# Performance work log

Measured on AMD Instinct MI355X. Metric: run time of the kernel, lower is better.

Reference implementation:

```python
import jax, jax.numpy as jnp
import numpy as np

T, H, I, E, Z, TOPK = 1024, 1024, 512, 32, 8, 4
ROUTED_SCALING = 1.0


def setup_inputs() -> dict:
    key = jax.random.key(0)
    k1, k2, k3, k4 = jax.random.split(key, 4)
    return {
        "hidden_states": jax.random.normal(k1, (T, H), jnp.float32),
        "router_w": jax.random.normal(k2, (E + Z, H), jnp.float32) * 0.02,
        "correction_bias": jnp.zeros((E + Z,), jnp.float32),
        "w_gate_up": jax.random.normal(k3, (E, 2 * I, H), jnp.float32) * 0.02,
        "w_down": jax.random.normal(k4, (E, H, I), jnp.float32) * 0.02,
        "top_k": TOPK,
    }


def reference(hidden_states, router_w, correction_bias, w_gate_up, w_down, top_k):
    # hidden_states: [T, H]; router_w: [E+Z, H]; w_gate_up: [E, 2I, H]; w_down: [E, H, I]
    t, h = hidden_states.shape
    e = w_gate_up.shape[0]
    i = w_down.shape[2]
    # --- router (float32, no bias; correction bias only affects selection) ---
    logits = jnp.einsum("th,eh->te", hidden_states.astype(jnp.float32), router_w)
    scores = jax.nn.softmax(logits, axis=-1)                     # [T, E+Z]
    _, idx = jax.lax.top_k(scores + correction_bias[None, :], top_k)  # [T, k]
    w = jnp.take_along_axis(scores, idx, axis=1) * ROUTED_SCALING     # renormalize=False
    # combine matrix [T, E+Z] (sparse top-k scattered dense)
    comb = jnp.zeros((t, scores.shape[1]), jnp.float32)
    comb = comb.at[jnp.arange(t)[:, None], idx].add(w)
    comb_routed = comb[:, :e].astype(hidden_states.dtype)        # [T, E]
    zero_w = comb[:, e:].sum(-1).astype(hidden_states.dtype)     # [T] identity zero-experts
    # --- grouped SiLU-gated expert MLPs (dense all-experts reference) ---
    gu = jnp.einsum("th,eih->eti", hidden_states, w_gate_up)     # [E, T, 2I]
    hmid = jax.nn.silu(gu[..., :i]) * gu[..., i:]                # [E, T, I]
    ye = jnp.einsum("eti,ehi->eth", hmid, w_down)                # [E, T, H]
    out = jnp.einsum("te,eth->th", comb_routed, ye)
    out = out + zero_w[:, None] * hidden_states
    return out
```

## Files before the change

kernel.cpp:

```cpp
#include <hip/hip_runtime.h>
#include <hip/hip_bf16.h>
#include <math.h>

#define TT   1024
#define HH   1024
#define II   512
#define EE   32
#define NE   40
#define TOPK 4
#define CAP  1024

#define GM  128
#define GK  32

typedef __attribute__((ext_vector_type(4))) short short4v;
typedef __attribute__((ext_vector_type(8))) short short8v;
typedef __attribute__((ext_vector_type(4))) float floatx4;

static __device__ __forceinline__ short f2bf(float f) {
    unsigned u = __float_as_uint(f);
    unsigned r = (u + 0x7fffu + ((u >> 16) & 1u)) >> 16;
    return (short)(r & 0xffffu);
}
static __device__ __forceinline__ float bf2f(short s) {
    return __uint_as_float(((unsigned)(unsigned short)s) << 16);
}
#if defined(__has_builtin)
#if __has_builtin(__builtin_amdgcn_cvt_pk_bf16_f32)
#define HAVE_PK_BF16 1
#endif
#endif
static __device__ __forceinline__ unsigned pk2(float a, float b) {
#ifdef HAVE_PK_BF16
    typedef __attribute__((ext_vector_type(2))) __bf16 bf2t;
    union { bf2t v; unsigned u; } cv;
    cv.v = __builtin_amdgcn_cvt_pk_bf16_f32(a, b);
    return cv.u;
#else
    return (unsigned)(unsigned short)f2bf(a) | ((unsigned)(unsigned short)f2bf(b) << 16);
#endif
}
static __device__ __forceinline__ short4v cvt4(float4 v) {
    union { unsigned u[2]; short4v s; } cv;
    cv.u[0] = pk2(v.x, v.y); cv.u[1] = pk2(v.z, v.w);
    return cv.s;
}
static __device__ __forceinline__ short8v pack8(float4 f0, float4 f1) {
    union { short4v h[2]; short8v v; } u;
    u.h[0] = cvt4(f0); u.h[1] = cvt4(f1);
    return u.v;
}


__global__ __launch_bounds__(256, 4) void kA(
    const float* __restrict__ x, const float* __restrict__ rw,
    const float* __restrict__ bias, float* __restrict__ topk_w,
    float* __restrict__ zero_w, int* __restrict__ kexp,
    short* __restrict__ xb)
{
    const int bx = blockIdx.x, tid = threadIdx.x;
    const int lane = tid & 63;
    const int w    = tid >> 6;

    if (w < 2) {
        const int t = bx * 2 + w;
        float xv[16];
        #pragma unroll
        for (int i = 0; i < 16; ++i) xv[i] = x[(size_t)t * HH + 64 * i + lane];

        float mylogit = -INFINITY;
        for (int e0 = 0; e0 < NE; e0 += 4) {
            const float* r0 = rw + (size_t)e0 * HH;
            float p[4] = { 0.f, 0.f, 0.f, 0.f };
            #pragma unroll
            for (int i = 0; i < 16; ++i) {
                int h = 64 * i + lane;
                #pragma unroll
                for (int j = 0; j < 4; ++j) p[j] += xv[i] * r0[(size_t)j * HH + h];
            }
            #pragma unroll
            for (int j = 0; j < 4; ++j) {
                #pragma unroll
                for (int off = 32; off > 0; off >>= 1) p[j] += __shfl_xor(p[j], off);
                if (lane == e0 + j) mylogit = p[j];
            }
        }

        float m = mylogit;
        #pragma unroll
        for (int off = 32; off > 0; off >>= 1) m = fmaxf(m, __shfl_xor(m, off));
        float pexp = (lane < NE) ? expf(mylogit - m) : 0.f;
        float s = pexp;
        #pragma unroll
        for (int off = 32; off > 0; off >>= 1) s += __shfl_xor(s, off);
        const float score = pexp / s;

        float val = (lane < NE) ? score + bias[lane] : -INFINITY;
        int   kidx[TOPK];
        float kw[TOPK];
        #pragma unroll
        for (int k = 0; k < TOPK; ++k) {
            float v = val; int idx = lane;
            #pragma unroll
            for (int off = 32; off > 0; off >>= 1) {
                float ov = __shfl_xor(v, off);
                int   oi = __shfl_xor(idx, off);
                if (ov > v || (ov == v && oi < idx)) { v = ov; idx = oi; }
            }
            kidx[k] = idx;
            kw[k]   = __shfl(score, idx);
            if (lane == idx) val = -INFINITY;
        }

        if (lane == 0) {
            float zw = 0.f;
            #pragma unroll
            for (int k = 0; k < TOPK; ++k) {
                int slot = t * TOPK + k;
                topk_w[slot] = kw[k];
                kexp[slot]   = kidx[k];
                if (kidx[k] >= EE) zw += kw[k];
            }
            zero_w[t] = zw;
        }
    } else {
        const int t = bx * 2 + (w - 2);
        const float4* xr = (const float4*)(x + (size_t)t * HH);
        short4v* xbr = (short4v*)(xb + (size_t)t * HH);
        #pragma unroll
        for (int i = 0; i < 4; ++i) xbr[lane + 64 * i] = cvt4(xr[lane + 64 * i]);
    }
}

__global__ __launch_bounds__(256, 4) void kA2(
    const int* __restrict__ kexp, int* __restrict__ counts,
    int* __restrict__ slots)
{
    __shared__ int wsum[4];
    __shared__ int base;
    const int e = blockIdx.x;
    const int tid = threadIdx.x, lane = tid & 63, w = tid >> 6;
    if (tid == 0) base = 0;
    __syncthreads();
    for (int i0 = 0; i0 < TT * TOPK; i0 += 256) {
        const int i = i0 + tid;
        const bool m = (kexp[i] == e);
        unsigned long long bal = __ballot(m);
        int pre  = __popcll(bal & ((1ull << lane) - 1ull));
        int wcnt = __popcll(bal);
        if (lane == 0) wsum[w] = wcnt;
        __syncthreads();
        int woff = 0;
        #pragma unroll
        for (int j = 0; j < 4; ++j) if (j < w) woff += wsum[j];
        const int tot = wsum[0] + wsum[1] + wsum[2] + wsum[3];
        if (m) slots[e * CAP + base + woff + pre] = i;
        __syncthreads();
        if (tid == 0) base += tot;
        __syncthreads();
    }
    if (tid == 0) counts[e] = base;
}

__global__ __launch_bounds__(256, 4) void kB(
    const short* __restrict__ xb, const float* __restrict__ wgu,
    const int* __restrict__ counts, const int* __restrict__ slots,
    const float* __restrict__ topk_w, short* __restrict__ hmid)
{
    __shared__ int   ssl[GM];
    __shared__ float swv[GM];
    const int bx = blockIdx.x, tid = threadIdx.x;
    const int e      = bx >> 5;
    const int c_base = (bx & 31) * 16;
    const int cnt    = counts[e];
    const float* wb  = wgu + (size_t)e * (2 * II) * HH;

    const int lane = tid & 63;
    const int w    = tid >> 6;
    const int quad = lane >> 4;
    const int mcol = lane & 15;
    constexpr int NT = HH / GK;

    const float* pG = wb + (size_t)(c_base + mcol) * HH + quad * 8;
    const float* pU = wb + (size_t)(II + c_base + mcol) * HH + quad * 8;

    for (int m_base = 0; m_base < cnt; m_base += GM) {
        __syncthreads();
        if (tid < GM) {
            int m = m_base + tid;
            int s = (m < cnt) ? slots[e * CAP + m] : -1;
            ssl[tid] = s;
            swv[tid] = (s >= 0) ? topk_w[s] : 0.f;
        }
        __syncthreads();

        const short *pA0, *pA1;
        {
            int s0 = ssl[w * 32 +      mcol];
            int s1 = ssl[w * 32 + 16 + mcol];
            pA0 = xb + (size_t)((s0 >= 0 ? s0 : 0) >> 2) * HH + quad * 8;
            pA1 = xb + (size_t)((s1 >= 0 ? s1 : 0) >> 2) * HH + quad * 8;
        }

        floatx4 accg0 = {}, accg1 = {}, accu0 = {}, accu1 = {};
        short8v aA0, aA1, aB0, aB1;
        float4  gA0, gA1, uA0, uA1, gB0, gB1, uB0, uB1;

        aA0 = *(const short8v*)(pA0);
        aA1 = *(const short8v*)(pA1);
        gA0 = *(const float4*)(pG);     gA1 = *(const float4*)(pG + 4);
        uA0 = *(const float4*)(pU);     uA1 = *(const float4*)(pU + 4);

        for (int t = 0; t < NT; t += 2) {
            const int k1 = (t + 1) * GK;
            aB0 = *(const short8v*)(pA0 + k1);
            aB1 = *(const short8v*)(pA1 + k1);
            gB0 = *(const float4*)(pG + k1); gB1 = *(const float4*)(pG + k1 + 4);
            uB0 = *(const float4*)(pU + k1); uB1 = *(const float4*)(pU + k1 + 4);
            {
                short8v bg = pack8(gA0, gA1), bu = pack8(uA0, uA1);
                accg0 = __builtin_amdgcn_mfma_f32_16x16x32_bf16(aA0, bg, accg0, 0, 0, 0);
                accu0 = __builtin_amdgcn_mfma_f32_16x16x32_bf16(aA0, bu, accu0, 0, 0, 0);
                accg1 = __builtin_amdgcn_mfma_f32_16x16x32_bf16(aA1, bg, accg1, 0, 0, 0);
                accu1 = __builtin_amdgcn_mfma_f32_16x16x32_bf16(aA1, bu, accu1, 0, 0, 0);
            }
            const int k2 = (t + 2) * GK;
            if (k2 < HH) {
                aA0 = *(const short8v*)(pA0 + k2);
                aA1 = *(const short8v*)(pA1 + k2);
                gA0 = *(const float4*)(pG + k2); gA1 = *(const float4*)(pG + k2 + 4);
                uA0 = *(const float4*)(pU + k2); uA1 = *(const float4*)(pU + k2 + 4);
            }
            {
                short8v bg = pack8(gB0, gB1), bu = pack8(uB0, uB1);
                accg0 = __builtin_amdgcn_mfma_f32_16x16x32_bf16(aB0, bg, accg0, 0, 0, 0);
                accu0 = __builtin_amdgcn_mfma_f32_16x16x32_bf16(aB0, bu, accu0, 0, 0, 0);
                accg1 = __builtin_amdgcn_mfma_f32_16x16x32_bf16(aB1, bg, accg1, 0, 0, 0);
                accu1 = __builtin_amdgcn_mfma_f32_16x16x32_bf16(aB1, bu, accu1, 0, 0, 0);
            }
        }

        #pragma unroll
        for (int r = 0; r < 4; ++r) {
            int m0 = w * 32 + quad * 4 + r;
            int s0 = ssl[m0];
            if (s0 >= 0) {
                float g = accg0[r], u = accu0[r];
                hmid[(size_t)s0 * II + c_base + mcol] =
                    f2bf(swv[m0] * g * u / (1.f + __expf(-g)));
            }
            int m1 = w * 32 + 16 + quad * 4 + r;
            int s1 = ssl[m1];
            if (s1 >= 0) {
                float g = accg1[r], u = accu1[r];
                hmid[(size_t)s1 * II + c_base + mcol] =
                    f2bf(swv[m1] * g * u / (1.f + __expf(-g)));
            }
        }
    }
}

__global__ __launch_bounds__(256, 4) void kC(
    const short* __restrict__ hmid, const float* __restrict__ wd,
    const int* __restrict__ counts, const int* __restrict__ slots,
    short* __restrict__ ydown)
{
    __shared__ int ssl[GM];
    const int bx = blockIdx.x, tid = threadIdx.x;
    const int e      = bx >> 5;
    const int n_base = (bx & 31) * 32;
    const int cnt    = counts[e];
    const float* wb  = wd + (size_t)e * HH * II;

    const int lane = tid & 63;
    const int w    = tid >> 6;
    const int quad = lane >> 4;
    const int mcol = lane & 15;
    constexpr int NT = II / GK;

    const float* pW0 = wb + (size_t)(n_base +      mcol) * II + quad * 8;
    const float* pW1 = wb + (size_t)(n_base + 16 + mcol) * II + quad * 8;

    for (int m_base = 0; m_base < cnt; m_base += GM) {
        __syncthreads();
        if (tid < GM) {
            int m = m_base + tid;
            ssl[tid] = (m < cnt) ? slots[e * CAP + m] : -1;
        }
        __syncthreads();

        const short *pA0, *pA1;
        {
            int s0 = ssl[w * 32 +      mcol];
            int s1 = ssl[w * 32 + 16 + mcol];
            pA0 = hmid + (size_t)(s0 >= 0 ? s0 : 0) * II + quad * 8;
            pA1 = hmid + (size_t)(s1 >= 0 ? s1 : 0) * II + quad * 8;
        }

        floatx4 acc00 = {}, acc01 = {}, acc10 = {}, acc11 = {};
        short8v aA0, aA1, aB0, aB1;
        float4  p0A, p1A, q0A, q1A, p0B, p1B, q0B, q1B;

        aA0 = *(const short8v*)(pA0);
        aA1 = *(const short8v*)(pA1);
        p0A = *(const float4*)(pW0);     p1A = *(const float4*)(pW0 + 4);
        q0A = *(const float4*)(pW1);     q1A = *(const float4*)(pW1 + 4);

        for (int t = 0; t < NT; t += 2) {
            const int k1 = (t + 1) * GK;
            aB0 = *(const short8v*)(pA0 + k1);
            aB1 = *(const short8v*)(pA1 + k1);
            p0B = *(const float4*)(pW0 + k1); p1B = *(const float4*)(pW0 + k1 + 4);
            q0B = *(const float4*)(pW1 + k1); q1B = *(const float4*)(pW1 + k1 + 4);
            {
                short8v b0 = pack8(p0A, p1A), b1 = pack8(q0A, q1A);
                acc00 = __builtin_amdgcn_mfma_f32_16x16x32_bf16(aA0, b0, acc00, 0, 0, 0);
                acc01 = __builtin_amdgcn_mfma_f32_16x16x32_bf16(aA0, b1, acc01, 0, 0, 0);
                acc10 = __builtin_amdgcn_mfma_f32_16x16x32_bf16(aA1, b0, acc10, 0, 0, 0);
                acc11 = __builtin_amdgcn_mfma_f32_16x16x32_bf16(aA1, b1, acc11, 0, 0, 0);
            }
            const int k2 = (t + 2) * GK;
            if (k2 < II) {
                aA0 = *(const short8v*)(pA0 + k2);
                aA1 = *(const short8v*)(pA1 + k2);
                p0A = *(const float4*)(pW0 + k2); p1A = *(const float4*)(pW0 + k2 + 4);
                q0A = *(const float4*)(pW1 + k2); q1A = *(const float4*)(pW1 + k2 + 4);
            }
            {
                short8v b0 = pack8(p0B, p1B), b1 = pack8(q0B, q1B);
                acc00 = __builtin_amdgcn_mfma_f32_16x16x32_bf16(aB0, b0, acc00, 0, 0, 0);
                acc01 = __builtin_amdgcn_mfma_f32_16x16x32_bf16(aB0, b1, acc01, 0, 0, 0);
                acc10 = __builtin_amdgcn_mfma_f32_16x16x32_bf16(aB1, b0, acc10, 0, 0, 0);
                acc11 = __builtin_amdgcn_mfma_f32_16x16x32_bf16(aB1, b1, acc11, 0, 0, 0);
            }
        }

        #pragma unroll
        for (int r = 0; r < 4; ++r) {
            int m0 = w * 32 + quad * 4 + r;
            int s0 = ssl[m0];
            if (s0 >= 0) {
                short* yrow = ydown + (size_t)s0 * HH + n_base;
                yrow[mcol]      = f2bf(acc00[r]);
                yrow[16 + mcol] = f2bf(acc01[r]);
            }
            int m1 = w * 32 + 16 + quad * 4 + r;
            int s1 = ssl[m1];
            if (s1 >= 0) {
                short* yrow = ydown + (size_t)s1 * HH + n_base;
                yrow[mcol]      = f2bf(acc10[r]);
                yrow[16 + mcol] = f2bf(acc11[r]);
            }
        }
    }
}

__global__ __launch_bounds__(256, 4) void kD(
    const float* __restrict__ x, const short* __restrict__ ydown,
    const int* __restrict__ kexp, const float* __restrict__ zero_w,
    float* __restrict__ out)
{
    const int bx = blockIdx.x, tid = threadIdx.x;
    const int t = bx;
    const float4 xvv = ((const float4*)(x + (size_t)t * HH))[tid];
    const float zw = zero_w[t];
    float4 o;
    o.x = zw * xvv.x; o.y = zw * xvv.y; o.z = zw * xvv.z; o.w = zw * xvv.w;
    #pragma unroll
    for (int k = 0; k < TOPK; ++k) {
        int slot = t * TOPK + k;
        if (kexp[slot] < EE) {
            short4v y = *(const short4v*)&ydown[(size_t)slot * HH + tid * 4];
            o.x += bf2f(y[0]); o.y += bf2f(y[1]);
            o.z += bf2f(y[2]); o.w += bf2f(y[3]);
        }
    }
    ((float4*)(out + (size_t)t * HH))[tid] = o;
}

extern "C" void kernel_launch(void* const* d_in, const int* in_sizes, int n_in,
                              void* d_out, int out_size, void* d_ws, size_t ws_size,
                              hipStream_t stream) {
    const float* x    = (const float*)d_in[0];
    const float* rw   = (const float*)d_in[1];
    const float* bias = (const float*)d_in[2];
    const float* wgu  = (const float*)d_in[3];
    const float* wd   = (const float*)d_in[4];
    float* out = (float*)d_out;

    char* ws = (char*)d_ws;
    int*   counts = (int*)ws;
    float* topk_w = (float*)(ws + 1024);
    float* zero_w = (float*)(ws + 17408);
    int*   kexp   = (int*)(ws + 21504);
    int*   slots  = (int*)(ws + 40960);
    short* xb     = (short*)(ws + 262144);
    short* hmid   = (short*)(ws + 2359296);
    short* ydown  = (short*)(ws + 6553600);

    kA <<<dim3(512),  dim3(256), 0, stream>>>(x, rw, bias, topk_w, zero_w, kexp, xb);
    kA2<<<dim3(32),   dim3(256), 0, stream>>>(kexp, counts, slots);
    kB <<<dim3(1024), dim3(256), 0, stream>>>(xb, wgu, counts, slots, topk_w, hmid);
    kC <<<dim3(1024), dim3(256), 0, stream>>>(hmid, wd, counts, slots, ydown);
    kD <<<dim3(1024), dim3(256), 0, stream>>>(x, ydown, kexp, zero_w, out);
}
```

Baseline: 351.2 us.

## Stage expert weight tiles through LDS with async global_load_lds multi-stage pipeline

In the gate/up and down-projection kernels, each wave used to load its fp32 weight fragments straight from global memory into registers. Now the whole block cooperatively streams weight tiles into an 8-slot swizzled LDS ring with global_load_lds, keeping six stages in flight and gating each step on vmcnt waits and barriers. Each block's weights are shared by its four waves, so the change aims to cut duplicate global traffic and hide memory latency. In exchange it adds 32KB of LDS per block, which may lower occupancy, plus a barrier every k-step, and the hand-counted vmcnt values must correctly cover the interleaved activation loads.

```diff
diff --git a/kernel.cpp b/kernel.cpp
--- a/kernel.cpp
+++ b/kernel.cpp
@@ -16,6 +16,8 @@
 typedef __attribute__((ext_vector_type(4))) short short4v;
 typedef __attribute__((ext_vector_type(8))) short short8v;
 typedef __attribute__((ext_vector_type(4))) float floatx4;
+
+#define FENCE() asm volatile("" ::: "memory")
 
 static __device__ __forceinline__ short f2bf(float f) {
     unsigned u = __float_as_uint(f);
@@ -49,6 +51,11 @@
     union { short4v h[2]; short8v v; } u;
     u.h[0] = cvt4(f0); u.h[1] = cvt4(f1);
     return u.v;
+}
+static __device__ __forceinline__ void gload_lds16(const float* g, float* l) {
+    __builtin_amdgcn_global_load_lds(
+        (const __attribute__((address_space(1))) unsigned int*)g,
+        (__attribute__((address_space(3))) unsigned int*)l, 16, 0, 0);
 }
 
 
@@ -167,6 +174,7 @@
     const int* __restrict__ counts, const int* __restrict__ slots,
     const float* __restrict__ topk_w, short* __restrict__ hmid)
 {
+    __shared__ float smB[8][1024];
     __shared__ int   ssl[GM];
     __shared__ float swv[GM];
     const int bx = blockIdx.x, tid = threadIdx.x;
@@ -181,8 +189,32 @@
     const int mcol = lane & 15;
     constexpr int NT = HH / GK;
 
-    const float* pG = wb + (size_t)(c_base + mcol) * HH + quad * 8;
-    const float* pU = wb + (size_t)(II + c_base + mcol) * HH + quad * 8;
+    const int srow  = tid >> 3;
+    const int spart = (tid & 7) ^ (srow & 7);
+    const int grow  = (srow < 16) ? (c_base + srow) : (II + c_base + (srow - 16));
+    const float* srcB = wb + (size_t)grow * HH + spart * 4;
+
+    const int swz  = (mcol & 7) << 4;
+    const int offG = ((mcol * 128 + quad * 32) ^ swz);
+    const int offU = (((16 + mcol) * 128 + quad * 32) ^ swz);
+
+#define STAGE_B(s) gload_lds16(srcB + (size_t)(s) * GK, &smB[(s) & 7][0] + w * 256)
+
+#define BODY_B(s, A0, A1, NSTR) do { \
+    asm volatile("s_waitcnt vmcnt(" NSTR ")" ::: "memory"); \
+    __builtin_amdgcn_s_barrier(); \
+    FENCE(); \
+    const char* bb = (const char*)&smB[(s) & 7][0]; \
+    float4 g0 = *(const float4*)(bb + offG); \
+    float4 g1 = *(const float4*)(bb + (offG ^ 16)); \
+    float4 u0 = *(const float4*)(bb + offU); \
+    float4 u1 = *(const float4*)(bb + (offU ^ 16)); \
+    short8v bg = pack8(g0, g1), bu = pack8(u0, u1); \
+    accg0 = __builtin_amdgcn_mfma_f32_16x16x32_bf16(A0, bg, accg0, 0, 0, 0); \
+    accu0 = __builtin_amdgcn_mfma_f32_16x16x32_bf16(A0, bu, accu0, 0, 0, 0); \
+    accg1 = __builtin_amdgcn_mfma_f32_16x16x32_bf16(A1, bg, accg1, 0, 0, 0); \
+    accu1 = __builtin_amdgcn_mfma_f32_16x16x32_bf16(A1, bu, accu1, 0, 0, 0); \
+} while (0)
 
     for (int m_base = 0; m_base < cnt; m_base += GM) {
         __syncthreads();
@@ -204,39 +236,35 @@
 
         floatx4 accg0 = {}, accg1 = {}, accu0 = {}, accu1 = {};
         short8v aA0, aA1, aB0, aB1;
-        float4  gA0, gA1, uA0, uA1, gB0, gB1, uB0, uB1;
-
+
+        STAGE_B(0); FENCE(); STAGE_B(1); FENCE(); STAGE_B(2); FENCE();
+        STAGE_B(3); FENCE(); STAGE_B(4); FENCE(); STAGE_B(5); FENCE();
         aA0 = *(const short8v*)(pA0);
         aA1 = *(const short8v*)(pA1);
-        gA0 = *(const float4*)(pG);     gA1 = *(const float4*)(pG + 4);
-        uA0 = *(const float4*)(pU);     uA1 = *(const float4*)(pU + 4);
-
-        for (int t = 0; t < NT; t += 2) {
-            const int k1 = (t + 1) * GK;
-            aB0 = *(const short8v*)(pA0 + k1);
-            aB1 = *(const short8v*)(pA1 + k1);
-            gB0 = *(const float4*)(pG + k1); gB1 = *(const float4*)(pG + k1 + 4);
-            uB0 = *(const float4*)(pU + k1); uB1 = *(const float4*)(pU + k1 + 4);
-            {
-                short8v bg = pack8(gA0, gA1), bu = pack8(uA0, uA1);
-                accg0 = __builtin_amdgcn_mfma_f32_16x16x32_bf16(aA0, bg, accg0, 0, 0, 0);
-                accu0 = __builtin_amdgcn_mfma_f32_16x16x32_bf16(aA0, bu, accu0, 0, 0, 0);
-                accg1 = __builtin_amdgcn_mfma_f32_16x16x32_bf16(aA1, bg, accg1, 0, 0, 0);
-                accu1 = __builtin_amdgcn_mfma_f32_16x16x32_bf16(aA1, bu, accu1, 0, 0, 0);
-            }
-            const int k2 = (t + 2) * GK;
-            if (k2 < HH) {
-                aA0 = *(const short8v*)(pA0 + k2);
-                aA1 = *(const short8v*)(pA1 + k2);
-                gA0 = *(const float4*)(pG + k2); gA1 = *(const float4*)(pG + k2 + 4);
-                uA0 = *(const float4*)(pU + k2); uA1 = *(const float4*)(pU + k2 + 4);
-            }
-            {
-                short8v bg = pack8(gB0, gB1), bu = pack8(uB0, uB1);
-                accg0 = __builtin_amdgcn_mfma_f32_16x16x32_bf16(aB0, bg, accg0, 0, 0, 0);
-                accu0 = __builtin_amdgcn_mfma_f32_16x16x32_bf16(aB0, bu, accu0, 0, 0, 0);
-                accg1 = __builtin_amdgcn_mfma_f32_16x16x32_bf16(aB1, bg, accg1, 0, 0, 0);
-                accu1 = __builtin_amdgcn_mfma_f32_16x16x32_bf16(aB1, bu, accu1, 0, 0, 0);
+        aB0 = *(const short8v*)(pA0 + GK);
+        aB1 = *(const short8v*)(pA1 + GK);
+        FENCE();
+
+        for (int s = 0; s < NT - 6; s += 2) {
+            BODY_B(s, aA0, aA1, "9");
+            aA0 = *(const short8v*)(pA0 + (s + 2) * GK);
+            aA1 = *(const short8v*)(pA1 + (s + 2) * GK);
+            STAGE_B(s + 6);
+            BODY_B(s + 1, aB0, aB1, "9");
+            aB0 = *(const short8v*)(pA0 + (s + 3) * GK);
+            aB1 = *(const short8v*)(pA1 + (s + 3) * GK);
+            STAGE_B(s + 7);
+        }
+        for (int s = NT - 6; s < NT; s += 2) {
+            BODY_B(s, aA0, aA1, "0");
+            if (s + 2 < NT) {
+                aA0 = *(const short8v*)(pA0 + (s + 2) * GK);
+                aA1 = *(const short8v*)(pA1 + (s + 2) * GK);
+            }
+            BODY_B(s + 1, aB0, aB1, "0");
+            if (s + 3 < NT) {
+                aB0 = *(const short8v*)(pA0 + (s + 3) * GK);
+                aB1 = *(const short8v*)(pA1 + (s + 3) * GK);
             }
         }
 
@@ -258,6 +286,8 @@
             }
         }
     }
+#undef STAGE_B
+#undef BODY_B
 }
 
 __global__ __launch_bounds__(256, 4) void kC(
@@ -265,7 +295,8 @@
     const int* __restrict__ counts, const int* __restrict__ slots,
     short* __restrict__ ydown)
 {
-    __shared__ int ssl[GM];
+    __shared__ float smC[8][1024];
+    __shared__ int   ssl[GM];
     const int bx = blockIdx.x, tid = threadIdx.x;
     const int e      = bx >> 5;
     const int n_base = (bx & 31) * 32;
@@ -278,8 +309,31 @@
     const int mcol = lane & 15;
     constexpr int NT = II / GK;
 
-    const float* pW0 = wb + (size_t)(n_base +      mcol) * II + quad * 8;
-    const float* pW1 = wb + (size_t)(n_base + 16 + mcol) * II + quad * 8;
+    const int srow  = tid >> 3;
+    const int spart = (tid & 7) ^ (srow & 7);
+    const float* srcB = wb + (size_t)(n_base + srow) * II + spart * 4;
+
+    const int swz  = (mcol & 7) << 4;
+    const int off0 = ((mcol * 128 + quad * 32) ^ swz);
+    const int off1 = (((16 + mcol) * 128 + quad * 32) ^ swz);
+
+#define STAGE_C(s) gload_lds16(srcB + (size_t)(s) * GK, &smC[(s) & 7][0] + w * 256)
+
+#define BODY_C(s, A0, A1, NSTR) do { \
+    asm volatile("s_waitcnt vmcnt(" NSTR ")" ::: "memory"); \
+    __builtin_amdgcn_s_barrier(); \
+    FENCE(); \
+    const char* bb = (const char*)&smC[(s) & 7][0]; \
+    float4 p0 = *(const float4*)(bb + off0); \
+    float4 p1 = *(const float4*)(bb + (off0 ^ 16)); \
+    float4 q0 = *(const float4*)(bb + off1); \
+    float4 q1 = *(const float4*)(bb + (off1 ^ 16)); \
+    short8v b0 = pack8(p0, p1), b1 = pack8(q0, q1); \
+    acc00 = __builtin_amdgcn_mfma_f32_16x16x32_bf16(A0, b0, acc00, 0, 0, 0); \
+    acc01 = __builtin_amdgcn_mfma_f32_16x16x32_bf16(A0, b1, acc01, 0, 0, 0); \
+    acc10 = __builtin_amdgcn_mfma_f32_16x16x32_bf16(A1, b0, acc10, 0, 0, 0); \
+    acc11 = __builtin_amdgcn_mfma_f32_16x16x32_bf16(A1, b1, acc11, 0, 0, 0); \
+} while (0)
 
     for (int m_base = 0; m_base < cnt; m_base += GM) {
         __syncthreads();
@@ -299,39 +353,35 @@
 
         floatx4 acc00 = {}, acc01 = {}, acc10 = {}, acc11 = {};
         short8v aA0, aA1, aB0, aB1;
-        float4  p0A, p1A, q0A, q1A, p0B, p1B, q0B, q1B;
-
+
+        STAGE_C(0); FENCE(); STAGE_C(1); FENCE(); STAGE_C(2); FENCE();
+        STAGE_C(3); FENCE(); STAGE_C(4); FENCE(); STAGE_C(5); FENCE();
         aA0 = *(const short8v*)(pA0);
         aA1 = *(const short8v*)(pA1);
-        p0A = *(const float4*)(pW0);     p1A = *(const float4*)(pW0 + 4);
-        q0A = *(const float4*)(pW1);     q1A = *(const float4*)(pW1 + 4);
-
-        for (int t = 0; t < NT; t += 2) {
-            const int k1 = (t + 1) * GK;
-            aB0 = *(const short8v*)(pA0 + k1);
-            aB1 = *(const short8v*)(pA1 + k1);
-            p0B = *(const float4*)(pW0 + k1); p1B = *(const float4*)(pW0 + k1 + 4);
-            q0B = *(const float4*)(pW1 + k1); q1B = *(const float4*)(pW1 + k1 + 4);
-            {
-                short8v b0 = pack8(p0A, p1A), b1 = pack8(q0A, q1A);
-                acc00 = __builtin_amdgcn_mfma_f32_16x16x32_bf16(aA0, b0, acc00, 0, 0, 0);
-                acc01 = __builtin_amdgcn_mfma_f32_16x16x32_bf16(aA0, b1, acc01, 0, 0, 0);
-                acc10 = __builtin_amdgcn_mfma_f32_16x16x32_bf16(aA1, b0, acc10, 0, 0, 0);
-                acc11 = __builtin_amdgcn_mfma_f32_16x16x32_bf16(aA1, b1, acc11, 0, 0, 0);
-            }
-            const int k2 = (t + 2) * GK;
-            if (k2 < II) {
-                aA0 = *(const short8v*)(pA0 + k2);
-                aA1 = *(const short8v*)(pA1 + k2);
-                p0A = *(const float4*)(pW0 + k2); p1A = *(const float4*)(pW0 + k2 + 4);
-                q0A = *(const float4*)(pW1 + k2); q1A = *(const float4*)(pW1 + k2 + 4);
-            }
-            {
-                short8v b0 = pack8(p0B, p1B), b1 = pack8(q0B, q1B);
-                acc00 = __builtin_amdgcn_mfma_f32_16x16x32_bf16(aB0, b0, acc00, 0, 0, 0);
-                acc01 = __builtin_amdgcn_mfma_f32_16x16x32_bf16(aB0, b1, acc01, 0, 0, 0);
-                acc10 = __builtin_amdgcn_mfma_f32_16x16x32_bf16(aB1, b0, acc10, 0, 0, 0);
-                acc11 = __builtin_amdgcn_mfma_f32_16x16x32_bf16(aB1, b1, acc11, 0, 0, 0);
+        aB0 = *(const short8v*)(pA0 + GK);
+        aB1 = *(const short8v*)(pA1 + GK);
+        FENCE();
+
+        for (int s = 0; s < NT - 6; s += 2) {
+            BODY_C(s, aA0, aA1, "9");
+            aA0 = *(const short8v*)(pA0 + (s + 2) * GK);
+            aA1 = *(const short8v*)(pA1 + (s + 2) * GK);
+            STAGE_C(s + 6);
+            BODY_C(s + 1, aB0, aB1, "9");
+            aB0 = *(const short8v*)(pA0 + (s + 3) * GK);
+            aB1 = *(const short8v*)(pA1 + (s + 3) * GK);
+            STAGE_C(s + 7);
+        }
+        for (int s = NT - 6; s < NT; s += 2) {
+            BODY_C(s, aA0, aA1, "0");
+            if (s + 2 < NT) {
+                aA0 = *(const short8v*)(pA0 + (s + 2) * GK);
+                aA1 = *(const short8v*)(pA1 + (s + 2) * GK);
+            }
+            BODY_C(s + 1, aB0, aB1, "0");
+            if (s + 3 < NT) {
+                aB0 = *(const short8v*)(pA0 + (s + 3) * GK);
+                aB1 = *(const short8v*)(pA1 + (s + 3) * GK);
             }
         }
 
@@ -353,6 +403,8 @@
             }
         }
     }
+#undef STAGE_C
+#undef BODY_C
 }
 
 __global__ __launch_bounds__(256, 4) void kD(
```

Result: faster. 311.1 us (-11.4%).
